# Kernel optimization log

Measured on AMD Instinct MI355X. Metric: run time of the kernel, lower is better.

The kernel has to match this reference:

```python
import jax, jax.numpy as jnp
import numpy as np

CODEBOOK_SIZE = 1024
CODE_DIM = 64
COMMITMENT_COST = 0.25
EMA_DECAY = 0.99
EPS = 1e-05


def setup_inputs() -> dict:
    key = jax.random.key(0)
    k1, k2, k3, k4 = jax.random.split(key, 4)
    z = jax.random.normal(k1, (16, 4096, CODE_DIM), dtype=jnp.float32)
    codebook = jax.random.normal(k2, (CODEBOOK_SIZE, CODE_DIM), dtype=jnp.float32)
    ema_cluster_size = jax.random.uniform(k3, (CODEBOOK_SIZE,), dtype=jnp.float32)
    ema_w = jax.random.normal(k4, (CODEBOOK_SIZE, CODE_DIM), dtype=jnp.float32)
    return {"z": z, "codebook": codebook, "ema_cluster_size": ema_cluster_size, "ema_w": ema_w}


def reference(z, codebook, ema_cluster_size, ema_w):
    B, T, D = z.shape
    K = CODEBOOK_SIZE
    z_flat = z.reshape(-1, D)  # [N, D]

    # Squared-distance expansion: ||z||^2 + ||c||^2 - 2 z c^T  -> [N, K]
    distances = (
        jnp.sum(z_flat * z_flat, axis=-1, keepdims=True)
        + jnp.sum(codebook * codebook, axis=-1)
        - 2.0 * jnp.matmul(z_flat, codebook.T)
    )
    indices = jnp.argmin(distances, axis=-1)  # [N]
    z_q = codebook[indices]  # [N, D] (gathered from OLD codebook)

    # --- EMA codebook update (training, no_grad in torch) ---
    ones = jnp.ones((z_flat.shape[0],), dtype=z_flat.dtype)
    cluster_size = jax.ops.segment_sum(ones, indices, num_segments=K)  # == one_hot.sum(0)
    cluster_sum = jax.ops.segment_sum(z_flat, indices, num_segments=K)  # == one_hot.T @ z_flat
    new_ecs = ema_cluster_size * EMA_DECAY + (1.0 - EMA_DECAY) * cluster_size
    new_ew = ema_w * EMA_DECAY + (1.0 - EMA_DECAY) * cluster_sum
    n = jnp.sum(new_ecs)
    cluster_size_stable = (new_ecs + EPS) / (n + K * EPS) * n
    new_codebook = new_ew / cluster_size_stable[:, None]

    # Commitment loss (EMA path): commitment_cost * mse(z_flat, stop_grad(z_q))
    commitment_loss = jnp.mean((z_flat - jax.lax.stop_gradient(z_q)) ** 2)
    vq_loss = COMMITMENT_COST * commitment_loss

    # Straight-through estimator
    z_q_st = z_flat + jax.lax.stop_gradient(z_q - z_flat)

    z_q_out = z_q_st.reshape(B, T, D)
    indices_out = indices.reshape(B, T)
    return (z_q_out, vq_loss, indices_out, new_codebook, new_ecs, new_ew)
```

## Files before the change

### kernel.cpp

```cpp
#include <hip/hip_runtime.h>

#define KC   1024
#define DD   64
#define NR   65536

#define DECAY     0.99f
#define ONEM      0.01f
#define EPSV      1e-5f
#define MARGIN_W  0.008f

#define OFF_ZQ    0
#define OFF_LOSS  4194304
#define OFF_IDX   4194305
#define OFF_NCB   4259841
#define OFF_NECS  4325377
#define OFF_NEW   4326401


typedef float  f32x4  __attribute__((ext_vector_type(4)));
typedef short  bf16x8 __attribute__((ext_vector_type(8)));

__device__ __forceinline__ unsigned short b16(float v) {
    union { float f; unsigned u; } x; x.f = v;
    return (unsigned short)((x.u + 0x7fffu + ((x.u >> 16) & 1u)) >> 16);
}
__device__ __forceinline__ float b2f(unsigned short h) {
    union { unsigned u; float f; } x; x.u = (unsigned)h << 16;
    return x.f;
}

__device__ __forceinline__ void gload_lds16(const void* g, void* l) {
    __builtin_amdgcn_global_load_lds(
        (const __attribute__((address_space(1))) unsigned int*)g,
        (__attribute__((address_space(3))) unsigned int*)l, 16, 0, 0);
}

__global__ void vq_prep(const float* __restrict__ cb, float* __restrict__ out,
                        unsigned short* __restrict__ cbh,
                        unsigned short* __restrict__ cbm,
                        float* __restrict__ cbT) {
    const int tid = blockIdx.x * blockDim.x + threadIdx.x;
    if (tid < 65536) {
        const int code = tid >> 6, d = tid & 63;
        const int g   = code >> 4, col = code & 15;
        const int kh  = d >> 5, hi2 = (d >> 3) & 3, e = d & 7;
        const int pi  = ((g * 2 + kh) * 64 + hi2 * 16 + col) * 8 + e;
        const float v = cb[tid];
        const unsigned short h = b16(v);
        cbh[pi] = h;
        cbm[pi] = b16(v - b2f(h));
        cbT[d * 1024 + code] = v;
    }
    if (tid < 1024) {
        const float4* c = reinterpret_cast<const float4*>(cb + tid * 64);
        float s = 0.f;
        #pragma unroll
        for (int j = 0; j < 16; ++j) {
            const float4 v = c[j];
            s += v.x*v.x + v.y*v.y + v.z*v.z + v.w*v.w;
        }
        out[OFF_NCB + tid] = s;
    }
    if (tid == 0) out[OFF_LOSS] = 0.0f;
}

__global__ __launch_bounds__(512, 6) void vq_main(const float* __restrict__ z,
                                                  const float* __restrict__ cc,
                                                  const unsigned short* __restrict__ cbh,
                                                  const unsigned short* __restrict__ cbm,
                                                  const float* __restrict__ cbT,
                                                  const float* __restrict__ cb,
                                                  unsigned short* __restrict__ idxw,
                                                  float* __restrict__ out) {
    const int t    = threadIdx.x;
    const int lane = t & 63;
    const int wid  = t >> 6;
    const int rowbase = blockIdx.x * 128;

    __shared__ char  ldsB[4][16384];
    __shared__ float s_cc[1024];
    __shared__ int   s_final[128];
    __shared__ int   s_flag[128];
    __shared__ float s_cd[8][32];
    __shared__ int   s_cix[8][32];
    __shared__ float s_red[8];
    __shared__ int   s_nflag;

    if (t == 0) s_nflag = 0;
    s_cc[t]       = cc[t];
    s_cc[t + 512] = cc[t + 512];

    #pragma unroll
    for (int c0 = 0; c0 < 2; ++c0) {
        const char* sh = (const char*)cbh + c0 * 8192 + wid * 1024 + lane * 16;
        const char* sm = (const char*)cbm + c0 * 8192 + wid * 1024 + lane * 16;
        gload_lds16(sh, &ldsB[c0][wid * 1024]);
        gload_lds16(sm, &ldsB[c0][8192 + wid * 1024]);
    }

    bf16x8 a0h, a0m, a1h, a1m;
    {
        const int ar = rowbase + wid * 16 + (lane & 15);
        const int kb = (lane >> 4) * 8;
        const float* zr = z + (size_t)ar * 64 + kb;
        const float4 v0a = *reinterpret_cast<const float4*>(zr);
        const float4 v0b = *reinterpret_cast<const float4*>(zr + 4);
        const float4 v1a = *reinterpret_cast<const float4*>(zr + 32);
        const float4 v1b = *reinterpret_cast<const float4*>(zr + 36);
        const float z0[8] = {v0a.x, v0a.y, v0a.z, v0a.w, v0b.x, v0b.y, v0b.z, v0b.w};
        const float z1[8] = {v1a.x, v1a.y, v1a.z, v1a.w, v1b.x, v1b.y, v1b.z, v1b.w};
        #pragma unroll
        for (int e = 0; e < 8; ++e) {
            const unsigned short h0 = b16(z0[e]);
            a0h[e] = (short)h0;
            a0m[e] = (short)b16(z0[e] - b2f(h0));
            const unsigned short h1 = b16(z1[e]);
            a1h[e] = (short)h1;
            a1m[e] = (short)b16(z1[e] - b2f(h1));
        }
    }
    asm volatile("s_waitcnt vmcnt(2)" ::: "memory");
    __builtin_amdgcn_s_barrier();
    __builtin_amdgcn_sched_barrier(0);

    const int lcol   = lane & 15;
    const int lane16 = lane * 16;

    float bd[4], b2v[4]; int bk[4];
    #pragma unroll
    for (int j = 0; j < 4; ++j) { bd[j] = 3.4e38f; b2v[j] = 3.4e38f; bk[j] = 0; }

    for (int c = 0; c < 16; ++c) {
        if (c + 2 < 16) {
            const char* sh = (const char*)cbh + (c + 2) * 8192 + wid * 1024 + lane * 16;
            const char* sm = (const char*)cbm + (c + 2) * 8192 + wid * 1024 + lane * 16;
            gload_lds16(sh, &ldsB[(c + 2) & 3][wid * 1024]);
            gload_lds16(sm, &ldsB[(c + 2) & 3][8192 + wid * 1024]);
        }
        const char* bh = ldsB[c & 3];
        const char* bm = ldsB[c & 3] + 8192;
        #pragma unroll
        for (int gl = 0; gl < 4; ++gl) {
            const bf16x8 bh0 = *reinterpret_cast<const bf16x8*>(bh + gl * 2048 + lane16);
            const bf16x8 bh1 = *reinterpret_cast<const bf16x8*>(bh + gl * 2048 + 1024 + lane16);
            const bf16x8 bm0 = *reinterpret_cast<const bf16x8*>(bm + gl * 2048 + lane16);
            const bf16x8 bm1 = *reinterpret_cast<const bf16x8*>(bm + gl * 2048 + 1024 + lane16);

            f32x4 p0 = {0.f, 0.f, 0.f, 0.f};
            f32x4 p1 = {0.f, 0.f, 0.f, 0.f};
            p0 = __builtin_amdgcn_mfma_f32_16x16x32_bf16(a0m, bh0, p0, 0, 0, 0);
            p1 = __builtin_amdgcn_mfma_f32_16x16x32_bf16(a1m, bh1, p1, 0, 0, 0);
            p0 = __builtin_amdgcn_mfma_f32_16x16x32_bf16(a0h, bm0, p0, 0, 0, 0);
            p1 = __builtin_amdgcn_mfma_f32_16x16x32_bf16(a1h, bm1, p1, 0, 0, 0);
            p0 = __builtin_amdgcn_mfma_f32_16x16x32_bf16(a0h, bh0, p0, 0, 0, 0);
            p1 = __builtin_amdgcn_mfma_f32_16x16x32_bf16(a1h, bh1, p1, 0, 0, 0);

            const float ccv = s_cc[(c * 4 + gl) * 16 + lcol];
            #pragma unroll
            for (int j = 0; j < 4; ++j) {
                const float s = fmaf(-2.f, p0[j] + p1[j], ccv);
                b2v[j] = __builtin_amdgcn_fmed3f(bd[j], s, b2v[j]);
                if (s < bd[j]) { bd[j] = s; bk[j] = (c * 4 + gl) * 16 + lcol; }
            }
        }
        if (c < 15) {
            if (c == 14) asm volatile("s_waitcnt vmcnt(0)" ::: "memory");
            else         asm volatile("s_waitcnt vmcnt(2)" ::: "memory");
            __builtin_amdgcn_s_barrier();
            __builtin_amdgcn_sched_barrier(0);
        }
    }

    #pragma unroll
    for (int m = 1; m < 16; m <<= 1) {
        #pragma unroll
        for (int j = 0; j < 4; ++j) {
            const float od = __shfl_xor(bd[j],  m);
            const int   oi = __shfl_xor(bk[j],  m);
            const float o2 = __shfl_xor(b2v[j], m);
            const float nb2 = fminf(fmaxf(bd[j], od), fminf(b2v[j], o2));
            if (od < bd[j] || (od == bd[j] && oi < bk[j])) { bd[j] = od; bk[j] = oi; }
            b2v[j] = nb2;
        }
    }
    if ((lane & 15) == 0) {
        #pragma unroll
        for (int j = 0; j < 4; ++j) {
            const int r = wid * 16 + ((lane >> 4) << 2) + j;
            s_final[r] = bk[j];
            if (b2v[j] - bd[j] < MARGIN_W) {
                const int p = atomicAdd(&s_nflag, 1);
                s_flag[p] = r;
            }
        }
    }
    __syncthreads();

    const int nf = s_nflag;
    for (int fb = 0; fb < nf; fb += 32) {
        const int ne = (nf - fb < 32) ? (nf - fb) : 32;
        {
            const int cbase = wid * 128;
            const int c0i = cbase + lane, c1i = c0i + 64;
            for (int i = 0; i < ne; ++i) {
                const int r = s_flag[fb + i];
                const float* zrow = z + (size_t)(rowbase + r) * 64;
                float a0 = 0.f, a1 = 0.f;
                #pragma unroll 8
                for (int d = 0; d < 64; ++d) {
                    const float zd = zrow[d];
                    const float* cr = cbT + d * 1024 + cbase + lane;
                    a0 = fmaf(zd, cr[0],  a0);
                    a1 = fmaf(zd, cr[64], a1);
                }
                float bd_ = fmaf(-2.f, a0, s_cc[c0i]); int bi_ = c0i;
                const float d1 = fmaf(-2.f, a1, s_cc[c1i]);
                if (d1 < bd_) { bd_ = d1; bi_ = c1i; }
                #pragma unroll
                for (int m = 32; m >= 1; m >>= 1) {
                    const float od = __shfl_xor(bd_, m);
                    const int   oi = __shfl_xor(bi_, m);
                    if (od < bd_ || (od == bd_ && oi < bi_)) { bd_ = od; bi_ = oi; }
                }
                if (lane == 0) { s_cd[wid][i] = bd_; s_cix[wid][i] = bi_; }
            }
        }
        __syncthreads();
        if (t < ne) {
            float bd_ = s_cd[0][t]; int bi_ = s_cix[0][t];
            #pragma unroll
            for (int w = 1; w < 8; ++w) {
                const float d = s_cd[w][t]; const int i2 = s_cix[w][t];
                if (d < bd_ || (d == bd_ && i2 < bi_)) { bd_ = d; bi_ = i2; }
            }
            s_final[s_flag[fb + t]] = bi_;
        }
        __syncthreads();
    }

    if (t < 128) {
        const int k2 = s_final[t];
        out[OFF_IDX + rowbase + t] = (float)k2;
        idxw[rowbase + t] = (unsigned short)k2;
    }

    float sse = 0.f;
    const float4* zb4 = reinterpret_cast<const float4*>(z) + (size_t)blockIdx.x * 2048;
    float4*       qb  = reinterpret_cast<float4*>(out + OFF_ZQ) + (size_t)blockIdx.x * 2048;
    const float4* cb4 = reinterpret_cast<const float4*>(cb);
    #pragma unroll
    for (int j = 0; j < 4; ++j) {
        const int f  = t + 512 * j;
        const int r  = f >> 4;
        const int fc = f & 15;
        const int gk = s_final[r];
        const float4 zv = zb4[f];
        const float4 cv = cb4[gk * 16 + fc];
        qb[f] = cv;
        const float e0 = zv.x - cv.x, e1 = zv.y - cv.y;
        const float e2 = zv.z - cv.z, e3 = zv.w - cv.w;
        sse += e0 * e0 + e1 * e1 + e2 * e2 + e3 * e3;
    }

    #pragma unroll
    for (int m = 32; m >= 1; m >>= 1) sse += __shfl_xor(sse, m);
    if (lane == 0) s_red[wid] = sse;
    __syncthreads();
    if (t == 0) {
        float tot = s_red[0];
        #pragma unroll
        for (int i = 1; i < 8; ++i) tot += s_red[i];
        atomicAdd(&out[OFF_LOSS], tot);
    }
}

__global__ __launch_bounds__(512) void vq_sums(const float* __restrict__ z,
                                               const unsigned short* __restrict__ idxw,
                                               float* __restrict__ psum,
                                               float* __restrict__ pcnt) {
    const int t    = threadIdx.x;
    const int lane = t & 63;
    const int w    = t >> 6;
    const int k    = blockIdx.x >> 3;
    const int of   = blockIdx.x & 7;
    const int base = of * 8192 + w * 1024;

    float acc = 0.f;
    int   c   = 0;

    typedef unsigned short u16x4 __attribute__((ext_vector_type(4)));
    const u16x4* ip = reinterpret_cast<const u16x4*>(idxw + base);
    u16x4 cur = ip[lane];
    for (int s = 0; s < 4; ++s) {
        u16x4 nxt = cur;
        if (s < 3) nxt = ip[(s + 1) * 64 + lane];
        const int r0 = base + s * 256;
        c += (cur[0] == k) + (cur[1] == k) + (cur[2] == k) + (cur[3] == k);
        unsigned long long m;
        m = __ballot(cur[0] == k);
        while (m) { const int j = __ffsll((long long)m) - 1; m &= m - 1;
                    acc += z[(size_t)(r0 + 4 * j + 0) * 64 + lane]; }
        m = __ballot(cur[1] == k);
        while (m) { const int j = __ffsll((long long)m) - 1; m &= m - 1;
                    acc += z[(size_t)(r0 + 4 * j + 1) * 64 + lane]; }
        m = __ballot(cur[2] == k);
        while (m) { const int j = __ffsll((long long)m) - 1; m &= m - 1;
                    acc += z[(size_t)(r0 + 4 * j + 2) * 64 + lane]; }
        m = __ballot(cur[3] == k);
        while (m) { const int j = __ffsll((long long)m) - 1; m &= m - 1;
                    acc += z[(size_t)(r0 + 4 * j + 3) * 64 + lane]; }
        cur = nxt;
    }

    #pragma unroll
    for (int m2 = 32; m2 >= 1; m2 >>= 1) c += __shfl_xor(c, m2);

    __shared__ float s_a[8][64];
    __shared__ int   s_c[8];
    if (lane == 0) s_c[w] = c;
    s_a[w][lane] = acc;
    __syncthreads();
    if (w == 0) {
        float s = s_a[0][lane];
        #pragma unroll
        for (int i = 1; i < 8; ++i) s += s_a[i][lane];
        psum[(size_t)of * 65536 + k * 64 + lane] = s;
        if (lane == 0) {
            int ct = s_c[0];
            #pragma unroll
            for (int i = 1; i < 8; ++i) ct += s_c[i];
            pcnt[of * 1024 + k] = (float)ct;
        }
    }
}

__global__ __launch_bounds__(1024) void vq_final(const float* __restrict__ ema_cs,
                                                 const float* __restrict__ ema_w,
                                                 const float* __restrict__ pcnt,
                                                 const float* __restrict__ psum,
                                                 float* __restrict__ out) {
    const int k = threadIdx.x;
    const int b = blockIdx.x;
    float cnt = pcnt[k];
    #pragma unroll
    for (int i = 1; i < 8; ++i) cnt += pcnt[i * 1024 + k];
    const float necs = DECAY * ema_cs[k] + ONEM * cnt;

    __shared__ float s_red[1024];
    __shared__ float s_den[1024];
    s_red[k] = necs;
    __syncthreads();
    for (int off = 512; off > 0; off >>= 1) {
        if (k < off) s_red[k] += s_red[k + off];
        __syncthreads();
    }
    const float n = s_red[0];
    s_den[k] = (necs + EPSV) / (n + (float)KC * EPSV) * n;
    if (k >= b * 16 && k < (b + 1) * 16) out[OFF_NECS + k] = necs;
    __syncthreads();

    const int e = b * 1024 + k;
    float s = psum[e];
    #pragma unroll
    for (int i = 1; i < 8; ++i) s += psum[(size_t)i * 65536 + e];
    const float ew = DECAY * ema_w[e] + ONEM * s;
    out[OFF_NEW + e] = ew;
    out[OFF_NCB + e] = ew / s_den[e >> 6];
    if (b == 0 && k == 0) out[OFF_LOSS] = 0.25f * out[OFF_LOSS] * (1.f / 4194304.f);
}

extern "C" void kernel_launch(void* const* d_in, const int* in_sizes, int n_in,
                              void* d_out, int out_size, void* d_ws, size_t ws_size,
                              hipStream_t stream) {
    const float* z   = (const float*)d_in[0];
    const float* cb  = (const float*)d_in[1];
    const float* ecs = (const float*)d_in[2];
    const float* ew  = (const float*)d_in[3];
    float* out = (float*)d_out;

    unsigned short* cbh  = (unsigned short*)d_ws;
    unsigned short* cbm  = (unsigned short*)((char*)d_ws + 131072);
    float*          cbT  = (float*)((char*)d_ws + 262144);
    unsigned short* idxw = (unsigned short*)((char*)d_ws + 524288);
    float*          pcnt = (float*)((char*)d_ws + 655360);
    float*          psum = (float*)((char*)d_ws + 688128);

    vq_prep <<<256,  256, 0, stream>>>(cb, out, cbh, cbm, cbT);
    vq_main <<<512,  512, 0, stream>>>(z, out + OFF_NCB, cbh, cbm, cbT, cb, idxw, out);
    vq_sums <<<8192, 512, 0, stream>>>(z, idxw, psum, pcnt);
    vq_final<<<64,  1024, 0, stream>>>(ecs, ew, pcnt, psum, out);
}
```

Measured before the change: 79.37 us.

## Replace per-code ballot scan with shared-memory atomic histogram for cluster sums

The cluster-sum kernel used to launch one block per (code, row-chunk) pair, and every block rescanned all indices in its chunk looking for its code. That is 8192 blocks each reading the whole index array. The new kernel launches 128 blocks, each owning a row range and a 4-wide slice of D. Each block streams its rows once and accumulates into a shared-memory bin table with atomics. This removes the redundant index rescans and the scattered z loads, at the cost of LDS atomic contention and only 128 blocks in flight.

```diff
diff --git a/kernel.cpp b/kernel.cpp
--- a/kernel.cpp
+++ b/kernel.cpp
@@ -278,59 +278,38 @@
                                                const unsigned short* __restrict__ idxw,
                                                float* __restrict__ psum,
                                                float* __restrict__ pcnt) {
-    const int t    = threadIdx.x;
-    const int lane = t & 63;
-    const int w    = t >> 6;
-    const int k    = blockIdx.x >> 3;
-    const int of   = blockIdx.x & 7;
-    const int base = of * 8192 + w * 1024;
-
-    float acc = 0.f;
-    int   c   = 0;
-
-    typedef unsigned short u16x4 __attribute__((ext_vector_type(4)));
-    const u16x4* ip = reinterpret_cast<const u16x4*>(idxw + base);
-    u16x4 cur = ip[lane];
-    for (int s = 0; s < 4; ++s) {
-        u16x4 nxt = cur;
-        if (s < 3) nxt = ip[(s + 1) * 64 + lane];
-        const int r0 = base + s * 256;
-        c += (cur[0] == k) + (cur[1] == k) + (cur[2] == k) + (cur[3] == k);
-        unsigned long long m;
-        m = __ballot(cur[0] == k);
-        while (m) { const int j = __ffsll((long long)m) - 1; m &= m - 1;
-                    acc += z[(size_t)(r0 + 4 * j + 0) * 64 + lane]; }
-        m = __ballot(cur[1] == k);
-        while (m) { const int j = __ffsll((long long)m) - 1; m &= m - 1;
-                    acc += z[(size_t)(r0 + 4 * j + 1) * 64 + lane]; }
-        m = __ballot(cur[2] == k);
-        while (m) { const int j = __ffsll((long long)m) - 1; m &= m - 1;
-                    acc += z[(size_t)(r0 + 4 * j + 2) * 64 + lane]; }
-        m = __ballot(cur[3] == k);
-        while (m) { const int j = __ffsll((long long)m) - 1; m &= m - 1;
-                    acc += z[(size_t)(r0 + 4 * j + 3) * 64 + lane]; }
-        cur = nxt;
-    }
-
-    #pragma unroll
-    for (int m2 = 32; m2 >= 1; m2 >>= 1) c += __shfl_xor(c, m2);
-
-    __shared__ float s_a[8][64];
-    __shared__ int   s_c[8];
-    if (lane == 0) s_c[w] = c;
-    s_a[w][lane] = acc;
-    __syncthreads();
-    if (w == 0) {
-        float s = s_a[0][lane];
-        #pragma unroll
-        for (int i = 1; i < 8; ++i) s += s_a[i][lane];
-        psum[(size_t)of * 65536 + k * 64 + lane] = s;
-        if (lane == 0) {
-            int ct = s_c[0];
-            #pragma unroll
-            for (int i = 1; i < 8; ++i) ct += s_c[i];
-            pcnt[of * 1024 + k] = (float)ct;
-        }
+    const int t  = threadIdx.x;
+    const int rg = blockIdx.x >> 4;
+    const int dg = blockIdx.x & 15;
+    const int rbase = rg * 8192;
+
+    __shared__ float bins[1024][4];
+    __shared__ int   cbin[1024];
+
+    float* bflat = &bins[0][0];
+    for (int i = t; i < 4096; i += 512) bflat[i] = 0.f;
+    if (dg == 0) { cbin[t] = 0; cbin[t + 512] = 0; }
+    __syncthreads();
+
+    for (int s = 0; s < 16; ++s) {
+        const int r = rbase + s * 512 + t;
+        const int k = idxw[r];
+        const float4 zv = *reinterpret_cast<const float4*>(z + (size_t)r * 64 + dg * 4);
+        atomicAdd(&bins[k][0], zv.x);
+        atomicAdd(&bins[k][1], zv.y);
+        atomicAdd(&bins[k][2], zv.z);
+        atomicAdd(&bins[k][3], zv.w);
+        if (dg == 0) atomicAdd(&cbin[k], 1);
+    }
+    __syncthreads();
+
+    for (int i = t; i < 4096; i += 512) {
+        const int code = i >> 2, j = i & 3;
+        psum[(size_t)rg * 65536 + code * 64 + dg * 4 + j] = bins[code][j];
+    }
+    if (dg == 0) {
+        pcnt[rg * 1024 + t]       = (float)cbin[t];
+        pcnt[rg * 1024 + t + 512] = (float)cbin[t + 512];
     }
 }
 
@@ -385,8 +364,8 @@
     float*          pcnt = (float*)((char*)d_ws + 655360);
     float*          psum = (float*)((char*)d_ws + 688128);
 
-    vq_prep <<<256,  256, 0, stream>>>(cb, out, cbh, cbm, cbT);
-    vq_main <<<512,  512, 0, stream>>>(z, out + OFF_NCB, cbh, cbm, cbT, cb, idxw, out);
-    vq_sums <<<8192, 512, 0, stream>>>(z, idxw, psum, pcnt);
-    vq_final<<<64,  1024, 0, stream>>>(ecs, ew, pcnt, psum, out);
-}
+    vq_prep <<<256, 256, 0, stream>>>(cb, out, cbh, cbm, cbT);
+    vq_main <<<512, 512, 0, stream>>>(z, out + OFF_NCB, cbh, cbm, cbT, cb, idxw, out);
+    vq_sums <<<128, 512, 0, stream>>>(z, idxw, psum, pcnt);
+    vq_final<<<64, 1024, 0, stream>>>(ecs, ew, pcnt, psum, out);
+}
```

Measured after the change: 100.8 us. +26.9%, slower.
